# Optimization experiments

Hardware: AMD Instinct MI355X
Metric: run time of the kernel (lower is better)

## Reference

```python
import jax, jax.numpy as jnp
import numpy as np

N, C, H, W = 4, 256, 64, 64
C_EMBED = C // 2  # 128

def setup_inputs() -> dict:
    key = jax.random.key(0)
    k1, k2, k3, k4 = jax.random.split(key, 4)
    x = jax.random.normal(k1, (N, C, H, W), dtype=jnp.float32)
    # 1x1 conv weights stored as [out_ch, in_ch] (torch Conv2d weight squeezed)
    theta_w = jax.random.normal(k2, (C_EMBED, C), dtype=jnp.float32) * 0.01
    phi_w = jax.random.normal(k3, (C_EMBED, C), dtype=jnp.float32) * 0.01
    proj_w = jax.random.normal(k4, (C, C), dtype=jnp.float32) * 0.01
    return {"x": x, "theta_w": theta_w, "phi_w": phi_w, "proj_w": proj_w}

def reference(x, theta_w, phi_w, proj_w):
    n, c, h, w = x.shape
    s = h * w
    xf = x.reshape(n, c, s)  # [n, c, s]
    theta = jnp.einsum('ec,ncs->nse', theta_w, xf)  # [n, s, e]
    phi = jnp.einsum('ec,ncs->nes', phi_w, xf)      # [n, e, s]
    scale = jnp.sqrt(jnp.float32(theta_w.shape[0]))
    f = jnp.einsum('nse,net->nst', theta, phi) / scale  # [n, s, s]
    f = jax.nn.softmax(f, axis=-1)
    y = jnp.einsum('nst,nct->ncs', f, xf)  # attend over g = x, -> [n, c, s]
    res = jnp.einsum('oc,ncs->nos', proj_w, y)  # 1x1 projection conv
    return x + res.reshape(n, c, h, w)
```

## Files before the change

kernel.cpp:

```cpp
#include <hip/hip_runtime.h>
#include <cstdint>
#include <cstddef>

#define NB 4
#define CH 256
#define SS 4096
#define EE 128
#define QSCALE 0.08838834764831845f

typedef __attribute__((ext_vector_type(8))) short bfrag;
typedef __attribute__((ext_vector_type(8))) unsigned short u16x8;
typedef __attribute__((ext_vector_type(8))) _Float16 h16x8;
typedef __attribute__((ext_vector_type(4))) float f32x4;

__device__ __forceinline__ unsigned short f2bf(float f) {
  union { float f; unsigned int u; } v; v.f = f;
  unsigned int u = v.u;
  unsigned int r = u + 0x7FFFu + ((u >> 16) & 1u);
  return (unsigned short)(r >> 16);
}

__device__ __forceinline__ void lds_barrier() {
  asm volatile("s_waitcnt lgkmcnt(0)" ::: "memory");
  __builtin_amdgcn_s_barrier();
}

__global__ __launch_bounds__(256) void cvt_w(
    const float* __restrict__ thw, const float* __restrict__ phw,
    const float* __restrict__ pw,
    unsigned short* __restrict__ thwb, unsigned short* __restrict__ phwb,
    unsigned short* __restrict__ pwb)
{
  const int nw4 = EE * CH / 4;
  const int np4 = CH * CH / 4;
  int i = blockIdx.x * 256 + threadIdx.x;
  const float* src; unsigned short* dst; int off;
  if      (i < nw4)           { src = thw; dst = thwb; off = i; }
  else if (i < 2 * nw4)       { src = phw; dst = phwb; off = i - nw4; }
  else if (i < 2 * nw4 + np4) { src = pw;  dst = pwb;  off = i - 2 * nw4; }
  else return;
  float4 v = reinterpret_cast<const float4*>(src)[off];
  ushort4 o;
  o.x = f2bf(v.x); o.y = f2bf(v.y); o.z = f2bf(v.z); o.w = f2bf(v.w);
  reinterpret_cast<ushort4*>(dst)[off] = o;
}

__global__ __launch_bounds__(512) void pass1_qk(
    const float* __restrict__ x,
    const unsigned short* __restrict__ thw,
    const unsigned short* __restrict__ phw,
    unsigned short* __restrict__ xb,
    unsigned short* __restrict__ Qt,
    unsigned short* __restrict__ Kt)
{
  __shared__ unsigned short xT[64][CH + 8];
  const int t  = threadIdx.x;
  const int n  = blockIdx.y;
  const int s0 = blockIdx.x * 64;

  {
    const int soff = (t & 15) * 4;
    const int c0   = t >> 4;
    #pragma unroll
    for (int ci = 0; ci < 8; ++ci) {
      const int c = c0 + ci * 32;
      const size_t rowoff = ((size_t)n * CH + c) * SS + s0;
      float4 v = reinterpret_cast<const float4*>(x + rowoff)[soff >> 2];
      ushort4 o;
      o.x = f2bf(v.x); o.y = f2bf(v.y); o.z = f2bf(v.z); o.w = f2bf(v.w);
      reinterpret_cast<ushort4*>(xb + rowoff)[soff >> 2] = o;
      xT[soff + 0][c] = o.x;
      xT[soff + 1][c] = o.y;
      xT[soff + 2][c] = o.z;
      xT[soff + 3][c] = o.w;
    }
  }
  __syncthreads();

  const int w    = t >> 6;
  const int lane = t & 63;
  const int q    = lane >> 4;
  const int mr   = lane & 15;
  const int wrow = (w & 3) * 16;
  const int half = w >> 2;

  bfrag a[8];
  {
    const bfrag* rp = reinterpret_cast<const bfrag*>(&xT[wrow + mr][0]);
    #pragma unroll
    for (int k = 0; k < 8; ++k) a[k] = rp[k * 4 + q];
  }

  const unsigned short* wsel = half ? phw : thw;
  unsigned short*       osel = half ? Kt  : Qt;
  const float           sc   = half ? 1.0f : QSCALE;
  const bfrag* wp = reinterpret_cast<const bfrag*>(wsel);
  #pragma unroll
  for (int nt = 0; nt < 8; ++nt) {
    f32x4 acc = {0.f, 0.f, 0.f, 0.f};
    #pragma unroll
    for (int k = 0; k < 8; ++k) {
      bfrag b = wp[(nt * 16 + mr) * (CH / 8) + k * 4 + q];
      acc = __builtin_amdgcn_mfma_f32_16x16x32_bf16(a[k], b, acc, 0, 0, 0);
    }
    #pragma unroll
    for (int i = 0; i < 4; ++i) {
      const int srow = s0 + wrow + q * 4 + i;
      osel[((size_t)n * SS + srow) * EE + nt * 16 + mr] = f2bf(acc[i] * sc);
    }
  }
}

__global__ __launch_bounds__(512, 2) void pass2a(
    const unsigned short* __restrict__ Qt,
    const unsigned short* __restrict__ Kt,
    const unsigned short* __restrict__ xb,
    _Float16* __restrict__ Opart,
    float* __restrict__ ML)
{
  __shared__ __align__(16) unsigned char SMEM[103936];
  float          (*S_lds)[132] = reinterpret_cast<float(*)[132]>(SMEM);
  unsigned short (*P_lds)[136] = reinterpret_cast<unsigned short(*)[136]>(SMEM + 67584);
  float* row_m     = reinterpret_cast<float*>(SMEM + 102400);
  float* row_l     = reinterpret_cast<float*>(SMEM + 102912);
  float* row_alpha = reinterpret_cast<float*>(SMEM + 103424);

  const int t     = threadIdx.x;
  const int id    = blockIdx.x;
  const int xcd   = id & 7;
  const int n     = xcd >> 1;
  const int h     = xcd & 1;
  const int qt    = id >> 3;
  const int s0    = qt * 128;
  const int kbase = h * 2048;

  const int w      = t >> 6;
  const int lane   = t & 63;
  const int q      = lane >> 4;
  const int mr     = lane & 15;
  const int colblk = w & 3;
  const int rb     = (w >> 2) * 64;

  if (t < 128) { row_m[t] = -INFINITY; row_l[t] = 0.f; }

  bfrag qa[4][4];
  #pragma unroll
  for (int ms = 0; ms < 4; ++ms) {
    const bfrag* rp = reinterpret_cast<const bfrag*>(
        Qt + ((size_t)n * SS + s0 + rb + ms * 16 + mr) * EE);
    #pragma unroll
    for (int k = 0; k < 4; ++k) qa[ms][k] = rp[k * 4 + q];
  }

  f32x4 o_accA[4][2], o_accB[4][2];
  #pragma unroll
  for (int ms = 0; ms < 4; ++ms)
    #pragma unroll
    for (int nt = 0; nt < 2; ++nt) {
      o_accA[ms][nt] = (f32x4){0.f, 0.f, 0.f, 0.f};
      o_accB[ms][nt] = (f32x4){0.f, 0.f, 0.f, 0.f};
    }

  __syncthreads();

  bfrag kb[4][2];
  #pragma unroll
  for (int nt = 0; nt < 2; ++nt) {
    const bfrag* rp = reinterpret_cast<const bfrag*>(
        Kt + ((size_t)n * SS + kbase + colblk * 32 + nt * 16 + mr) * EE);
    #pragma unroll
    for (int k = 0; k < 4; ++k) kb[k][nt] = rp[k * 4 + q];
  }

#define PV_HALF(OACC, RB)                                                    \
  do {                                                                       \
    _Pragma("unroll")                                                        \
    for (int ms = 0; ms < 4; ++ms) {                                         \
      float al[4];                                                           \
      _Pragma("unroll")                                                      \
      for (int i = 0; i < 4; ++i) al[i] = row_alpha[(RB) + ms*16 + q*4 + i]; \
      _Pragma("unroll")                                                      \
      for (int nt = 0; nt < 2; ++nt)                                         \
        _Pragma("unroll")                                                    \
        for (int i = 0; i < 4; ++i) OACC[ms][nt][i] *= al[i];                \
    }                                                                        \
    _Pragma("unroll")                                                        \
    for (int kk = 0; kk < 4; ++kk) {                                         \
      bfrag pa[4];                                                           \
      _Pragma("unroll")                                                      \
      for (int ms = 0; ms < 4; ++ms)                                         \
        pa[ms] = reinterpret_cast<const bfrag*>(                             \
            &P_lds[(RB) + ms * 16 + mr][0])[kk * 4 + q];                     \
      _Pragma("unroll")                                                      \
      for (int nt = 0; nt < 2; ++nt)                                         \
        _Pragma("unroll")                                                    \
        for (int ms = 0; ms < 4; ++ms)                                       \
          OACC[ms][nt] = __builtin_amdgcn_mfma_f32_16x16x32_bf16(            \
              pa[ms], vb[kk][nt], OACC[ms][nt], 0, 0, 0);                    \
    }                                                                        \
  } while (0)

  for (int t0 = 0; t0 < 2048; t0 += 128) {
    bfrag vb[4][2];
    #pragma unroll
    for (int nt = 0; nt < 2; ++nt) {
      const int c = w * 32 + nt * 16 + mr;
      const bfrag* vp = reinterpret_cast<const bfrag*>(
          xb + ((size_t)n * CH + c) * SS + kbase + t0);
      #pragma unroll
      for (int kk = 0; kk < 4; ++kk) vb[kk][nt] = vp[kk * 4 + q];
    }

    #pragma unroll
    for (int ms = 0; ms < 4; ++ms) {
      f32x4 acc0 = {0.f, 0.f, 0.f, 0.f};
      f32x4 acc1 = {0.f, 0.f, 0.f, 0.f};
      #pragma unroll
      for (int k = 0; k < 4; ++k) {
        acc0 = __builtin_amdgcn_mfma_f32_16x16x32_bf16(qa[ms][k], kb[k][0], acc0, 0, 0, 0);
        acc1 = __builtin_amdgcn_mfma_f32_16x16x32_bf16(qa[ms][k], kb[k][1], acc1, 0, 0, 0);
      }
      #pragma unroll
      for (int i = 0; i < 4; ++i) {
        S_lds[rb + ms * 16 + q * 4 + i][colblk * 32 + mr]      = acc0[i];
        S_lds[rb + ms * 16 + q * 4 + i][colblk * 32 + 16 + mr] = acc1[i];
      }
    }
    lds_barrier();

    if (t0 + 128 < 2048) {
      #pragma unroll
      for (int nt = 0; nt < 2; ++nt) {
        const bfrag* rp = reinterpret_cast<const bfrag*>(
            Kt + ((size_t)n * SS + kbase + t0 + 128 + colblk * 32 + nt * 16 + mr) * EE);
        #pragma unroll
        for (int k = 0; k < 4; ++k) kb[k][nt] = rp[k * 4 + q];
      }
    }

    #pragma unroll
    for (int sh = 0; sh < 2; ++sh) {
      const int r  = sh * 64 + (t >> 3);
      const int cg = t & 7;
      const float4* srow = reinterpret_cast<const float4*>(&S_lds[r][cg * 16]);
      float4 v0 = srow[0], v1 = srow[1], v2 = srow[2], v3 = srow[3];
      float vmax = fmaxf(fmaxf(fmaxf(v0.x, v0.y), fmaxf(v0.z, v0.w)),
                         fmaxf(fmaxf(v1.x, v1.y), fmaxf(v1.z, v1.w)));
      vmax = fmaxf(vmax, fmaxf(fmaxf(fmaxf(v2.x, v2.y), fmaxf(v2.z, v2.w)),
                               fmaxf(fmaxf(v3.x, v3.y), fmaxf(v3.z, v3.w))));
      vmax = fmaxf(vmax, __shfl_xor(vmax, 1, 8));
      vmax = fmaxf(vmax, __shfl_xor(vmax, 2, 8));
      vmax = fmaxf(vmax, __shfl_xor(vmax, 4, 8));
      const float m_old = row_m[r];
      const float m_new = fmaxf(m_old, vmax);

      float p[16];
      p[0]=__expf(v0.x-m_new); p[1]=__expf(v0.y-m_new); p[2]=__expf(v0.z-m_new); p[3]=__expf(v0.w-m_new);
      p[4]=__expf(v1.x-m_new); p[5]=__expf(v1.y-m_new); p[6]=__expf(v1.z-m_new); p[7]=__expf(v1.w-m_new);
      p[8]=__expf(v2.x-m_new); p[9]=__expf(v2.y-m_new); p[10]=__expf(v2.z-m_new); p[11]=__expf(v2.w-m_new);
      p[12]=__expf(v3.x-m_new); p[13]=__expf(v3.y-m_new); p[14]=__expf(v3.z-m_new); p[15]=__expf(v3.w-m_new);
      float sum = 0.f;
      u16x8 pk0, pk1;
      #pragma unroll
      for (int j = 0; j < 8; ++j) { sum += p[j];     pk0[j] = f2bf(p[j]); }
      #pragma unroll
      for (int j = 0; j < 8; ++j) { sum += p[8 + j]; pk1[j] = f2bf(p[8 + j]); }
      *reinterpret_cast<u16x8*>(&P_lds[r][cg * 16])     = pk0;
      *reinterpret_cast<u16x8*>(&P_lds[r][cg * 16 + 8]) = pk1;
      sum += __shfl_xor(sum, 1, 8);
      sum += __shfl_xor(sum, 2, 8);
      sum += __shfl_xor(sum, 4, 8);
      if (cg == 0) {
        const float al = __expf(m_old - m_new);
        row_alpha[r] = al;
        row_m[r]     = m_new;
        row_l[r]     = row_l[r] * al + sum;
      }
    }
    lds_barrier();

    PV_HALF(o_accA, 0);
    PV_HALF(o_accB, 64);
  }

  const size_t p = ((size_t)(n * 32 + qt)) * 2 + h;

#define EPI_HALF(OACC, RB)                                                   \
  do {                                                                       \
    _Pragma("unroll")                                                        \
    for (int ms = 0; ms < 4; ++ms) {                                         \
      float inv[4];                                                          \
      _Pragma("unroll")                                                      \
      for (int i = 0; i < 4; ++i)                                            \
        inv[i] = 1.0f / row_l[(RB) + ms * 16 + q * 4 + i];                   \
      _Pragma("unroll")                                                      \
      for (int nt = 0; nt < 2; ++nt)                                         \
        _Pragma("unroll")                                                    \
        for (int i = 0; i < 4; ++i) {                                        \
          const size_t oi =                                                  \
              (p * 128 + (RB) + ms * 16 + q * 4 + i) * 256 +                 \
              w * 32 + nt * 16 + mr;                                         \
          Opart[oi] = (_Float16)(OACC[ms][nt][i] * inv[i]);                  \
        }                                                                    \
    }                                                                        \
  } while (0)

  EPI_HALF(o_accA, 0);
  EPI_HALF(o_accB, 64);
  if (t < 128) {
    ML[p * 256 + t * 2]     = row_m[t];
    ML[p * 256 + t * 2 + 1] = row_l[t];
  }
}

__global__ __launch_bounds__(512) void pass2b(
    const _Float16* __restrict__ Opart,
    const float* __restrict__ ML,
    const unsigned short* __restrict__ pwb,
    const float* __restrict__ x,
    float* __restrict__ out)
{
  __shared__ __align__(16) unsigned char SMEM[34816];
  unsigned short (*Y_lds)[CH + 8] =
      reinterpret_cast<unsigned short(*)[CH + 8]>(SMEM);
  float* w0 = reinterpret_cast<float*>(SMEM + 33792);
  float* w1 = reinterpret_cast<float*>(SMEM + 34048);

  const int t   = threadIdx.x;
  const int id  = blockIdx.x;
  const int n   = id >> 6;
  const int sub = id & 63;
  const int s0  = sub * 64;
  const int qt  = sub >> 1;
  const int rb  = (sub & 1) * 64;
  const size_t p0 = ((size_t)(n * 32 + qt)) * 2;

  if (t < 64) {
    const float ma = ML[p0 * 256 + (rb + t) * 2];
    const float la = ML[p0 * 256 + (rb + t) * 2 + 1];
    const float mb = ML[(p0 + 1) * 256 + (rb + t) * 2];
    const float lb = ML[(p0 + 1) * 256 + (rb + t) * 2 + 1];
    const float m  = fmaxf(ma, mb);
    const float e0 = __expf(ma - m) * la;
    const float e1 = __expf(mb - m) * lb;
    const float iL = 1.0f / (e0 + e1);
    w0[t] = e0 * iL;
    w1[t] = e1 * iL;
  }
  __syncthreads();

  {
    const int r = t >> 3;
    #pragma unroll
    for (int seg = 0; seg < 4; ++seg) {
      const int c0 = (t & 7) * 8 + seg * 64;
      const size_t ai = (p0 * 128 + rb + r) * 256 + c0;
      const size_t bi = ((p0 + 1) * 128 + rb + r) * 256 + c0;
      h16x8 ha = *reinterpret_cast<const h16x8*>(Opart + ai);
      h16x8 hb = *reinterpret_cast<const h16x8*>(Opart + bi);
      u16x8 y;
      #pragma unroll
      for (int j = 0; j < 8; ++j)
        y[j] = f2bf((float)ha[j] * w0[r] + (float)hb[j] * w1[r]);
      *reinterpret_cast<u16x8*>(&Y_lds[r][c0]) = y;
    }
  }
  __syncthreads();

  const int w    = t >> 6;
  const int lane = t & 63;
  const int q    = lane >> 4;
  const int mr   = lane & 15;
  #pragma unroll
  for (int ot = 0; ot < 2; ++ot) {
    const int o0 = w * 32 + ot * 16;
    bfrag a[8];
    {
      const bfrag* ap = reinterpret_cast<const bfrag*>(pwb + (o0 + mr) * CH);
      #pragma unroll
      for (int k = 0; k < 8; ++k) a[k] = ap[k * 4 + q];
    }
    #pragma unroll
    for (int st = 0; st < 4; ++st) {
      f32x4 acc = {0.f, 0.f, 0.f, 0.f};
      const bfrag* bp = reinterpret_cast<const bfrag*>(&Y_lds[st * 16 + mr][0]);
      #pragma unroll
      for (int k = 0; k < 8; ++k)
        acc = __builtin_amdgcn_mfma_f32_16x16x32_bf16(a[k], bp[k * 4 + q], acc, 0, 0, 0);
      #pragma unroll
      for (int i = 0; i < 4; ++i) {
        const int o = o0 + q * 4 + i;
        const int s = s0 + st * 16 + mr;
        const size_t idx = ((size_t)n * CH + o) * SS + s;
        out[idx] = x[idx] + acc[i];
      }
    }
  }
}

__global__ __launch_bounds__(512, 2) void pass2_full(
    const unsigned short* __restrict__ Qt,
    const unsigned short* __restrict__ Kt,
    const unsigned short* __restrict__ xb,
    const unsigned short* __restrict__ pwb,
    const float* __restrict__ x,
    float* __restrict__ out)
{
  __shared__ __align__(16) unsigned char SMEM[51968];
  float          (*S_lds)[132] = reinterpret_cast<float(*)[132]>(SMEM);
  unsigned short (*P_lds)[136] = reinterpret_cast<unsigned short(*)[136]>(SMEM + 33792);
  float* row_m     = reinterpret_cast<float*>(SMEM + 51200);
  float* row_l     = reinterpret_cast<float*>(SMEM + 51456);
  float* row_alpha = reinterpret_cast<float*>(SMEM + 51712);

  const int t    = threadIdx.x;
  const int id   = blockIdx.x;
  const int xcd  = id & 7;
  const int n    = xcd >> 1;
  const int s0   = ((id >> 3) * 2 + (xcd & 1)) * 64;
  const int w    = t >> 6;
  const int lane = t & 63;
  const int q    = lane >> 4;
  const int mr   = lane & 15;

  if (t < 64) { row_m[t] = -INFINITY; row_l[t] = 0.f; }

  bfrag qa[4][4];
  #pragma unroll
  for (int ms = 0; ms < 4; ++ms) {
    const bfrag* rp = reinterpret_cast<const bfrag*>(
        Qt + ((size_t)n * SS + s0 + ms * 16 + mr) * EE);
    #pragma unroll
    for (int k = 0; k < 4; ++k) qa[ms][k] = rp[k * 4 + q];
  }

  f32x4 o_acc[4][2];
  #pragma unroll
  for (int ms = 0; ms < 4; ++ms)
    #pragma unroll
    for (int nt = 0; nt < 2; ++nt) o_acc[ms][nt] = (f32x4){0.f, 0.f, 0.f, 0.f};

  bfrag kb[4];
  {
    const bfrag* rp = reinterpret_cast<const bfrag*>(
        Kt + ((size_t)n * SS + w * 16 + mr) * EE);
    #pragma unroll
    for (int k = 0; k < 4; ++k) kb[k] = rp[k * 4 + q];
  }

  for (int t0 = 0; t0 < SS; t0 += 128) {
    bfrag vb[4][2];
    #pragma unroll
    for (int nt = 0; nt < 2; ++nt) {
      const int c = w * 32 + nt * 16 + mr;
      const bfrag* vp = reinterpret_cast<const bfrag*>(
          xb + ((size_t)n * CH + c) * SS + t0);
      #pragma unroll
      for (int kk = 0; kk < 4; ++kk) vb[kk][nt] = vp[kk * 4 + q];
    }

    #pragma unroll
    for (int ms = 0; ms < 4; ++ms) {
      f32x4 acc = {0.f, 0.f, 0.f, 0.f};
      #pragma unroll
      for (int k = 0; k < 4; ++k)
        acc = __builtin_amdgcn_mfma_f32_16x16x32_bf16(qa[ms][k], kb[k], acc, 0, 0, 0);
      #pragma unroll
      for (int i = 0; i < 4; ++i)
        S_lds[ms * 16 + q * 4 + i][w * 16 + mr] = acc[i];
    }
    lds_barrier();

    {
      const int t1 = t0 + 128;
      if (t1 < SS) {
        const bfrag* rp = reinterpret_cast<const bfrag*>(
            Kt + ((size_t)n * SS + t1 + w * 16 + mr) * EE);
        #pragma unroll
        for (int k = 0; k < 4; ++k) kb[k] = rp[k * 4 + q];
      }
    }

    {
      const int r  = t >> 3;
      const int cg = t & 7;
      const float4* srow = reinterpret_cast<const float4*>(&S_lds[r][cg * 16]);
      float4 v0 = srow[0], v1 = srow[1], v2 = srow[2], v3 = srow[3];
      float vmax = fmaxf(fmaxf(fmaxf(v0.x, v0.y), fmaxf(v0.z, v0.w)),
                         fmaxf(fmaxf(v1.x, v1.y), fmaxf(v1.z, v1.w)));
      vmax = fmaxf(vmax, fmaxf(fmaxf(fmaxf(v2.x, v2.y), fmaxf(v2.z, v2.w)),
                               fmaxf(fmaxf(v3.x, v3.y), fmaxf(v3.z, v3.w))));
      vmax = fmaxf(vmax, __shfl_xor(vmax, 1, 8));
      vmax = fmaxf(vmax, __shfl_xor(vmax, 2, 8));
      vmax = fmaxf(vmax, __shfl_xor(vmax, 4, 8));
      const float m_old = row_m[r];
      const float m_new = fmaxf(m_old, vmax);

      float p[16];
      p[0]=__expf(v0.x-m_new); p[1]=__expf(v0.y-m_new); p[2]=__expf(v0.z-m_new); p[3]=__expf(v0.w-m_new);
      p[4]=__expf(v1.x-m_new); p[5]=__expf(v1.y-m_new); p[6]=__expf(v1.z-m_new); p[7]=__expf(v1.w-m_new);
      p[8]=__expf(v2.x-m_new); p[9]=__expf(v2.y-m_new); p[10]=__expf(v2.z-m_new); p[11]=__expf(v2.w-m_new);
      p[12]=__expf(v3.x-m_new); p[13]=__expf(v3.y-m_new); p[14]=__expf(v3.z-m_new); p[15]=__expf(v3.w-m_new);
      float sum = 0.f;
      u16x8 pk0, pk1;
      #pragma unroll
      for (int j = 0; j < 8; ++j) { sum += p[j];     pk0[j] = f2bf(p[j]); }
      #pragma unroll
      for (int j = 0; j < 8; ++j) { sum += p[8 + j]; pk1[j] = f2bf(p[8 + j]); }
      *reinterpret_cast<u16x8*>(&P_lds[r][cg * 16])     = pk0;
      *reinterpret_cast<u16x8*>(&P_lds[r][cg * 16 + 8]) = pk1;
      sum += __shfl_xor(sum, 1, 8);
      sum += __shfl_xor(sum, 2, 8);
      sum += __shfl_xor(sum, 4, 8);
      if (cg == 0) {
        const float al = __expf(m_old - m_new);
        row_alpha[r] = al;
        row_m[r]     = m_new;
        row_l[r]     = row_l[r] * al + sum;
      }
    }
    lds_barrier();

    #pragma unroll
    for (int ms = 0; ms < 4; ++ms) {
      float al[4];
      #pragma unroll
      for (int i = 0; i < 4; ++i) al[i] = row_alpha[ms * 16 + q * 4 + i];
      #pragma unroll
      for (int nt = 0; nt < 2; ++nt)
        #pragma unroll
        for (int i = 0; i < 4; ++i) o_acc[ms][nt][i] *= al[i];
    }

    #pragma unroll
    for (int kk = 0; kk < 4; ++kk) {
      bfrag pa[4];
      #pragma unroll
      for (int ms = 0; ms < 4; ++ms)
        pa[ms] = reinterpret_cast<const bfrag*>(&P_lds[ms * 16 + mr][0])[kk * 4 + q];
      #pragma unroll
      for (int nt = 0; nt < 2; ++nt)
        #pragma unroll
        for (int ms = 0; ms < 4; ++ms)
          o_acc[ms][nt] = __builtin_amdgcn_mfma_f32_16x16x32_bf16(
              pa[ms], vb[kk][nt], o_acc[ms][nt], 0, 0, 0);
    }
  }

  __syncthreads();
  unsigned short (*Y_lds)[CH + 8] =
      reinterpret_cast<unsigned short(*)[CH + 8]>(SMEM);

  #pragma unroll
  for (int ms = 0; ms < 4; ++ms) {
    float inv[4];
    #pragma unroll
    for (int i = 0; i < 4; ++i) inv[i] = 1.0f / row_l[ms * 16 + q * 4 + i];
    #pragma unroll
    for (int nt = 0; nt < 2; ++nt) {
      const int c = w * 32 + nt * 16 + mr;
      #pragma unroll
      for (int i = 0; i < 4; ++i)
        Y_lds[ms * 16 + q * 4 + i][c] = f2bf(o_acc[ms][nt][i] * inv[i]);
    }
  }
  __syncthreads();

  #pragma unroll
  for (int ot = 0; ot < 2; ++ot) {
    const int o0 = w * 32 + ot * 16;
    bfrag a[8];
    {
      const bfrag* ap = reinterpret_cast<const bfrag*>(pwb + (o0 + mr) * CH);
      #pragma unroll
      for (int k = 0; k < 8; ++k) a[k] = ap[k * 4 + q];
    }
    #pragma unroll
    for (int st = 0; st < 4; ++st) {
      f32x4 acc = {0.f, 0.f, 0.f, 0.f};
      const bfrag* bp = reinterpret_cast<const bfrag*>(&Y_lds[st * 16 + mr][0]);
      #pragma unroll
      for (int k = 0; k < 8; ++k)
        acc = __builtin_amdgcn_mfma_f32_16x16x32_bf16(a[k], bp[k * 4 + q], acc, 0, 0, 0);
      #pragma unroll
      for (int i = 0; i < 4; ++i) {
        const int o = o0 + q * 4 + i;
        const int s = s0 + st * 16 + mr;
        const size_t idx = ((size_t)n * CH + o) * SS + s;
        out[idx] = x[idx] + acc[i];
      }
    }
  }
}

extern "C" void kernel_launch(void* const* d_in, const int* in_sizes, int n_in,
                              void* d_out, int out_size, void* d_ws, size_t ws_size,
                              hipStream_t stream) {
  const float* x   = (const float*)d_in[0];
  const float* thw = (const float*)d_in[1];
  const float* phw = (const float*)d_in[2];
  const float* pw  = (const float*)d_in[3];
  float* out = (float*)d_out;

  unsigned short* xb   = (unsigned short*)d_ws;
  unsigned short* Qt   = xb + (size_t)NB * CH * SS;
  unsigned short* Kt   = Qt + (size_t)NB * SS * EE;
  unsigned short* thwb = Kt + (size_t)NB * SS * EE;
  unsigned short* phwb = thwb + EE * CH;
  unsigned short* pwb  = phwb + EE * CH;
  float*          ML   = (float*)(pwb + CH * CH);
  _Float16*       Opart = (_Float16*)(ML + (size_t)256 * 128 * 2);

  const size_t opart_off = (size_t)((char*)Opart - (char*)d_ws);
  const size_t opart_bytes = (size_t)256 * 128 * 256 * 2;
  const int fits = ws_size >= opart_off + opart_bytes;

  const int nw4 = EE * CH / 4;
  const int np4 = CH * CH / 4;
  const int totw4 = 2 * nw4 + np4;
  cvt_w<<<(totw4 + 255) / 256, 256, 0, stream>>>(thw, phw, pw, thwb, phwb, pwb);

  pass1_qk<<<dim3(SS / 64, NB), 512, 0, stream>>>(x, thwb, phwb, xb, Qt, Kt);

  if (fits) {
    pass2a<<<dim3(256), 512, 0, stream>>>(Qt, Kt, xb, Opart, ML);
    pass2b<<<dim3(256), 512, 0, stream>>>(Opart, ML, pwb, x, out);
  } else {
    pass2_full<<<dim3(NB * SS / 64), 512, 0, stream>>>(Qt, Kt, xb, pwb, x, out);
  }
}
```

Before: 191.8 us.

## Split attention keys into quarters, stage Q/K in LDS, store scores as bf16

The flash-attention pass now splits the key range into four quarters instead of two, so it launches 512 blocks instead of 256. Q and K tiles are staged in LDS, with K double-buffered through registers, and the key step shrinks from 128 to 64. Scores are written to LDS as bf16 in a buffer shared with P, which cuts LDS use enough to allow higher occupancy (launch bounds 4). The combine kernel merges four partial results, which doubles the Opart workspace and its traffic, and rounding scores to bf16 before softmax costs accuracy.

```diff
diff --git a/kernel.cpp b/kernel.cpp
--- a/kernel.cpp
+++ b/kernel.cpp
@@ -18,6 +18,10 @@
   unsigned int u = v.u;
   unsigned int r = u + 0x7FFFu + ((u >> 16) & 1u);
   return (unsigned short)(r >> 16);
+}
+__device__ __forceinline__ float bf2f(unsigned short u) {
+  union { unsigned int u; float f; } v; v.u = ((unsigned int)u) << 16;
+  return v.f;
 }
 
 __device__ __forceinline__ void lds_barrier() {
@@ -111,45 +115,57 @@
   }
 }
 
-__global__ __launch_bounds__(512, 2) void pass2a(
+__global__ __launch_bounds__(512, 4) void pass2a(
     const unsigned short* __restrict__ Qt,
     const unsigned short* __restrict__ Kt,
     const unsigned short* __restrict__ xb,
     _Float16* __restrict__ Opart,
     float* __restrict__ ML)
 {
-  __shared__ __align__(16) unsigned char SMEM[103936];
-  float          (*S_lds)[132] = reinterpret_cast<float(*)[132]>(SMEM);
-  unsigned short (*P_lds)[136] = reinterpret_cast<unsigned short(*)[136]>(SMEM + 67584);
-  float* row_m     = reinterpret_cast<float*>(SMEM + 102400);
-  float* row_l     = reinterpret_cast<float*>(SMEM + 102912);
-  float* row_alpha = reinterpret_cast<float*>(SMEM + 103424);
-
-  const int t     = threadIdx.x;
-  const int id    = blockIdx.x;
-  const int xcd   = id & 7;
-  const int n     = xcd >> 1;
-  const int h     = xcd & 1;
-  const int qt    = id >> 3;
-  const int s0    = qt * 128;
-  const int kbase = h * 2048;
-
-  const int w      = t >> 6;
-  const int lane   = t & 63;
-  const int q      = lane >> 4;
-  const int mr     = lane & 15;
-  const int colblk = w & 3;
-  const int rb     = (w >> 2) * 64;
+  __shared__ __align__(16) unsigned char SMEM[69632];
+  unsigned short (*Q_lds)[132] = reinterpret_cast<unsigned short(*)[132]>(SMEM);
+  unsigned short (*SP)[68]     = reinterpret_cast<unsigned short(*)[68]>(SMEM + 33792);
+  unsigned short (*K_lds)[132] = reinterpret_cast<unsigned short(*)[132]>(SMEM + 51200);
+  float* row_m     = reinterpret_cast<float*>(SMEM + 68096);
+  float* row_l     = reinterpret_cast<float*>(SMEM + 68608);
+  float* row_alpha = reinterpret_cast<float*>(SMEM + 69120);
+
+  const int t       = threadIdx.x;
+  const int id      = blockIdx.x;
+  const int xcd     = id & 7;
+  const int n       = xcd >> 1;
+  const int quarter = (xcd & 1) * 2 + ((id >> 3) & 1);
+  const int qt      = id >> 4;
+  const int s0      = qt * 128;
+  const int kq0     = quarter * 1024;
+
+  const int w    = t >> 6;
+  const int lane = t & 63;
+  const int q    = lane >> 4;
+  const int mr   = lane & 15;
+  const int rb   = (w >> 2) * 64;
+  const int c4   = w & 3;
 
   if (t < 128) { row_m[t] = -INFINITY; row_l[t] = 0.f; }
 
-  bfrag qa[4][4];
-  #pragma unroll
-  for (int ms = 0; ms < 4; ++ms) {
-    const bfrag* rp = reinterpret_cast<const bfrag*>(
-        Qt + ((size_t)n * SS + s0 + rb + ms * 16 + mr) * EE);
-    #pragma unroll
-    for (int k = 0; k < 4; ++k) qa[ms][k] = rp[k * 4 + q];
+  {
+    const int r  = t >> 2;
+    const int j0 = (t & 3) * 4;
+    const unsigned short* src = Qt + ((size_t)n * SS + s0 + r) * EE;
+    #pragma unroll
+    for (int j = 0; j < 4; ++j) {
+      const int col = (j0 + j) * 8;
+      *reinterpret_cast<u16x8*>(&Q_lds[r][col]) =
+          *reinterpret_cast<const u16x8*>(src + col);
+    }
+  }
+  {
+    const int key = t >> 3, c = t & 7;
+    const unsigned short* src = Kt + ((size_t)n * SS + kq0 + key) * EE;
+    *reinterpret_cast<u16x8*>(&K_lds[key][c * 8]) =
+        *reinterpret_cast<const u16x8*>(src + c * 8);
+    *reinterpret_cast<u16x8*>(&K_lds[key][(c + 8) * 8]) =
+        *reinterpret_cast<const u16x8*>(src + (c + 8) * 8);
   }
 
   f32x4 o_accA[4][2], o_accB[4][2];
@@ -162,15 +178,6 @@
     }
 
   __syncthreads();
-
-  bfrag kb[4][2];
-  #pragma unroll
-  for (int nt = 0; nt < 2; ++nt) {
-    const bfrag* rp = reinterpret_cast<const bfrag*>(
-        Kt + ((size_t)n * SS + kbase + colblk * 32 + nt * 16 + mr) * EE);
-    #pragma unroll
-    for (int k = 0; k < 4; ++k) kb[k][nt] = rp[k * 4 + q];
-  }
 
 #define PV_HALF(OACC, RB)                                                    \
   do {                                                                       \
@@ -185,12 +192,12 @@
         for (int i = 0; i < 4; ++i) OACC[ms][nt][i] *= al[i];                \
     }                                                                        \
     _Pragma("unroll")                                                        \
-    for (int kk = 0; kk < 4; ++kk) {                                         \
+    for (int kk = 0; kk < 2; ++kk) {                                         \
       bfrag pa[4];                                                           \
       _Pragma("unroll")                                                      \
       for (int ms = 0; ms < 4; ++ms)                                         \
-        pa[ms] = reinterpret_cast<const bfrag*>(                             \
-            &P_lds[(RB) + ms * 16 + mr][0])[kk * 4 + q];                     \
+        pa[ms] = *reinterpret_cast<const bfrag*>(                            \
+            &SP[(RB) + ms * 16 + mr][(kk * 4 + q) * 8]);                     \
       _Pragma("unroll")                                                      \
       for (int nt = 0; nt < 2; ++nt)                                         \
         _Pragma("unroll")                                                    \
@@ -200,76 +207,78 @@
     }                                                                        \
   } while (0)
 
-  for (int t0 = 0; t0 < 2048; t0 += 128) {
-    bfrag vb[4][2];
+  for (int t0 = 0; t0 < 1024; t0 += 64) {
+    bfrag vb[2][2];
     #pragma unroll
     for (int nt = 0; nt < 2; ++nt) {
       const int c = w * 32 + nt * 16 + mr;
       const bfrag* vp = reinterpret_cast<const bfrag*>(
-          xb + ((size_t)n * CH + c) * SS + kbase + t0);
-      #pragma unroll
-      for (int kk = 0; kk < 4; ++kk) vb[kk][nt] = vp[kk * 4 + q];
-    }
-
-    #pragma unroll
-    for (int ms = 0; ms < 4; ++ms) {
-      f32x4 acc0 = {0.f, 0.f, 0.f, 0.f};
-      f32x4 acc1 = {0.f, 0.f, 0.f, 0.f};
-      #pragma unroll
-      for (int k = 0; k < 4; ++k) {
-        acc0 = __builtin_amdgcn_mfma_f32_16x16x32_bf16(qa[ms][k], kb[k][0], acc0, 0, 0, 0);
-        acc1 = __builtin_amdgcn_mfma_f32_16x16x32_bf16(qa[ms][k], kb[k][1], acc1, 0, 0, 0);
-      }
-      #pragma unroll
-      for (int i = 0; i < 4; ++i) {
-        S_lds[rb + ms * 16 + q * 4 + i][colblk * 32 + mr]      = acc0[i];
-        S_lds[rb + ms * 16 + q * 4 + i][colblk * 32 + 16 + mr] = acc1[i];
+          xb + ((size_t)n * CH + c) * SS + kq0 + t0);
+      vb[0][nt] = vp[q];
+      vb[1][nt] = vp[4 + q];
+    }
+
+    {
+      bfrag kb[4];
+      #pragma unroll
+      for (int k = 0; k < 4; ++k)
+        kb[k] = *reinterpret_cast<const bfrag*>(
+            &K_lds[c4 * 16 + mr][(k * 4 + q) * 8]);
+      #pragma unroll
+      for (int ms = 0; ms < 4; ++ms) {
+        f32x4 acc = {0.f, 0.f, 0.f, 0.f};
+        #pragma unroll
+        for (int k = 0; k < 4; ++k) {
+          bfrag aq = *reinterpret_cast<const bfrag*>(
+              &Q_lds[rb + ms * 16 + mr][(k * 4 + q) * 8]);
+          acc = __builtin_amdgcn_mfma_f32_16x16x32_bf16(aq, kb[k], acc, 0, 0, 0);
+        }
+        #pragma unroll
+        for (int i = 0; i < 4; ++i)
+          SP[rb + ms * 16 + q * 4 + i][c4 * 16 + mr] = f2bf(acc[i]);
       }
     }
     lds_barrier();
 
-    if (t0 + 128 < 2048) {
-      #pragma unroll
-      for (int nt = 0; nt < 2; ++nt) {
-        const bfrag* rp = reinterpret_cast<const bfrag*>(
-            Kt + ((size_t)n * SS + kbase + t0 + 128 + colblk * 32 + nt * 16 + mr) * EE);
-        #pragma unroll
-        for (int k = 0; k < 4; ++k) kb[k][nt] = rp[k * 4 + q];
-      }
-    }
-
-    #pragma unroll
-    for (int sh = 0; sh < 2; ++sh) {
-      const int r  = sh * 64 + (t >> 3);
-      const int cg = t & 7;
-      const float4* srow = reinterpret_cast<const float4*>(&S_lds[r][cg * 16]);
-      float4 v0 = srow[0], v1 = srow[1], v2 = srow[2], v3 = srow[3];
-      float vmax = fmaxf(fmaxf(fmaxf(v0.x, v0.y), fmaxf(v0.z, v0.w)),
-                         fmaxf(fmaxf(v1.x, v1.y), fmaxf(v1.z, v1.w)));
-      vmax = fmaxf(vmax, fmaxf(fmaxf(fmaxf(v2.x, v2.y), fmaxf(v2.z, v2.w)),
-                               fmaxf(fmaxf(v3.x, v3.y), fmaxf(v3.z, v3.w))));
-      vmax = fmaxf(vmax, __shfl_xor(vmax, 1, 8));
-      vmax = fmaxf(vmax, __shfl_xor(vmax, 2, 8));
-      vmax = fmaxf(vmax, __shfl_xor(vmax, 4, 8));
+    u16x8 kr0, kr1;
+    const bool pf = (t0 + 64) < 1024;
+    if (pf) {
+      const int key = t >> 3, c = t & 7;
+      const unsigned short* src =
+          Kt + ((size_t)n * SS + kq0 + t0 + 64 + key) * EE;
+      kr0 = *reinterpret_cast<const u16x8*>(src + c * 8);
+      kr1 = *reinterpret_cast<const u16x8*>(src + (c + 8) * 8);
+    }
+
+    {
+      const int r  = t >> 2;
+      const int cg = t & 3;
+      u16x8 sv0 = *reinterpret_cast<const u16x8*>(&SP[r][cg * 16]);
+      u16x8 sv1 = *reinterpret_cast<const u16x8*>(&SP[r][cg * 16 + 8]);
+      float s[16];
+      #pragma unroll
+      for (int j = 0; j < 8; ++j) { s[j] = bf2f(sv0[j]); s[8 + j] = bf2f(sv1[j]); }
+      float vmax = s[0];
+      #pragma unroll
+      for (int j = 1; j < 16; ++j) vmax = fmaxf(vmax, s[j]);
+      vmax = fmaxf(vmax, __shfl_xor(vmax, 1, 4));
+      vmax = fmaxf(vmax, __shfl_xor(vmax, 2, 4));
       const float m_old = row_m[r];
       const float m_new = fmaxf(m_old, vmax);
-
-      float p[16];
-      p[0]=__expf(v0.x-m_new); p[1]=__expf(v0.y-m_new); p[2]=__expf(v0.z-m_new); p[3]=__expf(v0.w-m_new);
-      p[4]=__expf(v1.x-m_new); p[5]=__expf(v1.y-m_new); p[6]=__expf(v1.z-m_new); p[7]=__expf(v1.w-m_new);
-      p[8]=__expf(v2.x-m_new); p[9]=__expf(v2.y-m_new); p[10]=__expf(v2.z-m_new); p[11]=__expf(v2.w-m_new);
-      p[12]=__expf(v3.x-m_new); p[13]=__expf(v3.y-m_new); p[14]=__expf(v3.z-m_new); p[15]=__expf(v3.w-m_new);
       float sum = 0.f;
       u16x8 pk0, pk1;
       #pragma unroll
-      for (int j = 0; j < 8; ++j) { sum += p[j];     pk0[j] = f2bf(p[j]); }
-      #pragma unroll
-      for (int j = 0; j < 8; ++j) { sum += p[8 + j]; pk1[j] = f2bf(p[8 + j]); }
-      *reinterpret_cast<u16x8*>(&P_lds[r][cg * 16])     = pk0;
-      *reinterpret_cast<u16x8*>(&P_lds[r][cg * 16 + 8]) = pk1;
-      sum += __shfl_xor(sum, 1, 8);
-      sum += __shfl_xor(sum, 2, 8);
-      sum += __shfl_xor(sum, 4, 8);
+      for (int j = 0; j < 8; ++j) {
+        float p = __expf(s[j] - m_new); sum += p; pk0[j] = f2bf(p);
+      }
+      #pragma unroll
+      for (int j = 0; j < 8; ++j) {
+        float p = __expf(s[8 + j] - m_new); sum += p; pk1[j] = f2bf(p);
+      }
+      *reinterpret_cast<u16x8*>(&SP[r][cg * 16])     = pk0;
+      *reinterpret_cast<u16x8*>(&SP[r][cg * 16 + 8]) = pk1;
+      sum += __shfl_xor(sum, 1, 4);
+      sum += __shfl_xor(sum, 2, 4);
       if (cg == 0) {
         const float al = __expf(m_old - m_new);
         row_alpha[r] = al;
@@ -281,9 +290,16 @@
 
     PV_HALF(o_accA, 0);
     PV_HALF(o_accB, 64);
-  }
-
-  const size_t p = ((size_t)(n * 32 + qt)) * 2 + h;
+
+    if (pf) {
+      const int key = t >> 3, c = t & 7;
+      *reinterpret_cast<u16x8*>(&K_lds[key][c * 8])       = kr0;
+      *reinterpret_cast<u16x8*>(&K_lds[key][(c + 8) * 8]) = kr1;
+    }
+    lds_barrier();
+  }
+
+  const size_t p = ((size_t)(n * 32 + qt)) * 4 + quarter;
 
 #define EPI_HALF(OACC, RB)                                                   \
   do {                                                                       \
@@ -323,8 +339,7 @@
   __shared__ __align__(16) unsigned char SMEM[34816];
   unsigned short (*Y_lds)[CH + 8] =
       reinterpret_cast<unsigned short(*)[CH + 8]>(SMEM);
-  float* w0 = reinterpret_cast<float*>(SMEM + 33792);
-  float* w1 = reinterpret_cast<float*>(SMEM + 34048);
+  float (*W)[64] = reinterpret_cast<float(*)[64]>(SMEM + 33792);
 
   const int t   = threadIdx.x;
   const int id  = blockIdx.x;
@@ -333,19 +348,22 @@
   const int s0  = sub * 64;
   const int qt  = sub >> 1;
   const int rb  = (sub & 1) * 64;
-  const size_t p0 = ((size_t)(n * 32 + qt)) * 2;
+  const size_t p0 = ((size_t)(n * 32 + qt)) * 4;
 
   if (t < 64) {
-    const float ma = ML[p0 * 256 + (rb + t) * 2];
-    const float la = ML[p0 * 256 + (rb + t) * 2 + 1];
-    const float mb = ML[(p0 + 1) * 256 + (rb + t) * 2];
-    const float lb = ML[(p0 + 1) * 256 + (rb + t) * 2 + 1];
-    const float m  = fmaxf(ma, mb);
-    const float e0 = __expf(ma - m) * la;
-    const float e1 = __expf(mb - m) * lb;
-    const float iL = 1.0f / (e0 + e1);
-    w0[t] = e0 * iL;
-    w1[t] = e1 * iL;
+    float m[4], l[4];
+    #pragma unroll
+    for (int qi = 0; qi < 4; ++qi) {
+      m[qi] = ML[(p0 + qi) * 256 + (rb + t) * 2];
+      l[qi] = ML[(p0 + qi) * 256 + (rb + t) * 2 + 1];
+    }
+    const float mm = fmaxf(fmaxf(m[0], m[1]), fmaxf(m[2], m[3]));
+    float e[4], se = 0.f;
+    #pragma unroll
+    for (int qi = 0; qi < 4; ++qi) { e[qi] = __expf(m[qi] - mm) * l[qi]; se += e[qi]; }
+    const float iL = 1.0f / se;
+    #pragma unroll
+    for (int qi = 0; qi < 4; ++qi) W[qi][t] = e[qi] * iL;
   }
   __syncthreads();
 
@@ -354,14 +372,18 @@
     #pragma unroll
     for (int seg = 0; seg < 4; ++seg) {
       const int c0 = (t & 7) * 8 + seg * 64;
-      const size_t ai = (p0 * 128 + rb + r) * 256 + c0;
-      const size_t bi = ((p0 + 1) * 128 + rb + r) * 256 + c0;
-      h16x8 ha = *reinterpret_cast<const h16x8*>(Opart + ai);
-      h16x8 hb = *reinterpret_cast<const h16x8*>(Opart + bi);
+      float acc[8] = {0.f, 0.f, 0.f, 0.f, 0.f, 0.f, 0.f, 0.f};
+      #pragma unroll
+      for (int qi = 0; qi < 4; ++qi) {
+        h16x8 hv = *reinterpret_cast<const h16x8*>(
+            Opart + ((p0 + qi) * 128 + rb + r) * 256 + c0);
+        const float wq = W[qi][r];
+        #pragma unroll
+        for (int j = 0; j < 8; ++j) acc[j] += (float)hv[j] * wq;
+      }
       u16x8 y;
       #pragma unroll
-      for (int j = 0; j < 8; ++j)
-        y[j] = f2bf((float)ha[j] * w0[r] + (float)hb[j] * w1[r]);
+      for (int j = 0; j < 8; ++j) y[j] = f2bf(acc[j]);
       *reinterpret_cast<u16x8*>(&Y_lds[r][c0]) = y;
     }
   }
@@ -609,10 +631,10 @@
   unsigned short* phwb = thwb + EE * CH;
   unsigned short* pwb  = phwb + EE * CH;
   float*          ML   = (float*)(pwb + CH * CH);
-  _Float16*       Opart = (_Float16*)(ML + (size_t)256 * 128 * 2);
-
-  const size_t opart_off = (size_t)((char*)Opart - (char*)d_ws);
-  const size_t opart_bytes = (size_t)256 * 128 * 256 * 2;
+  _Float16*       Opart = (_Float16*)(ML + (size_t)512 * 256);
+
+  const size_t opart_off  = (size_t)((char*)Opart - (char*)d_ws);
+  const size_t opart_bytes = (size_t)512 * 128 * 256 * 2;
   const int fits = ws_size >= opart_off + opart_bytes;
 
   const int nw4 = EE * CH / 4;
@@ -623,7 +645,7 @@
   pass1_qk<<<dim3(SS / 64, NB), 512, 0, stream>>>(x, thwb, phwb, xb, Qt, Kt);
 
   if (fits) {
-    pass2a<<<dim3(256), 512, 0, stream>>>(Qt, Kt, xb, Opart, ML);
+    pass2a<<<dim3(512), 512, 0, stream>>>(Qt, Kt, xb, Opart, ML);
     pass2b<<<dim3(256), 512, 0, stream>>>(Opart, ML, pwb, x, out);
   } else {
     pass2_full<<<dim3(NB * SS / 64), 512, 0, stream>>>(Qt, Kt, xb, pwb, x, out);
```

Result: slower. 425.8 us (+122.0%).

## Restructure attention pass to per-wave query rows with register softmax and LDS-staged V

Applied to the files above, without the earlier changes.

Reworks the flash-attention kernel so each wave owns 16 query rows and computes S transposed (K·Q) in registers. Row max, exp and sum are then done with cross-lane shuffles instead of round-tripping S and P through LDS. P fragments are rearranged into MFMA A-operand layout with shuffles. V (x) tiles of 64 keys are double-buffered in a swizzled LDS layout with a global prefetch, and there is one barrier per step instead of two. This cuts LDS traffic and synchronisation, at the cost of each wave reloading K from global memory, more MFMA steps with smaller key tiles, and 16 accumulator tiles of register pressure per wave.

```diff
diff --git a/kernel.cpp b/kernel.cpp
--- a/kernel.cpp
+++ b/kernel.cpp
@@ -18,6 +18,9 @@
   unsigned int u = v.u;
   unsigned int r = u + 0x7FFFu + ((u >> 16) & 1u);
   return (unsigned short)(r >> 16);
+}
+__device__ __forceinline__ unsigned int packbf(float a, float b) {
+  return (unsigned int)f2bf(a) | ((unsigned int)f2bf(b) << 16);
 }
 
 __device__ __forceinline__ void lds_barrier() {
@@ -118,12 +121,7 @@
     _Float16* __restrict__ Opart,
     float* __restrict__ ML)
 {
-  __shared__ __align__(16) unsigned char SMEM[103936];
-  float          (*S_lds)[132] = reinterpret_cast<float(*)[132]>(SMEM);
-  unsigned short (*P_lds)[136] = reinterpret_cast<unsigned short(*)[136]>(SMEM + 67584);
-  float* row_m     = reinterpret_cast<float*>(SMEM + 102400);
-  float* row_l     = reinterpret_cast<float*>(SMEM + 102912);
-  float* row_alpha = reinterpret_cast<float*>(SMEM + 103424);
+  __shared__ __align__(16) unsigned char SMEM[65536];
 
   const int t     = threadIdx.x;
   const int id    = blockIdx.x;
@@ -134,182 +132,174 @@
   const int s0    = qt * 128;
   const int kbase = h * 2048;
 
-  const int w      = t >> 6;
-  const int lane   = t & 63;
-  const int q      = lane >> 4;
-  const int mr     = lane & 15;
-  const int colblk = w & 3;
-  const int rb     = (w >> 2) * 64;
-
-  if (t < 128) { row_m[t] = -INFINITY; row_l[t] = 0.f; }
-
-  bfrag qa[4][4];
+  const int w    = t >> 6;
+  const int lane = t & 63;
+  const int q    = lane >> 4;
+  const int mr   = lane & 15;
+  const int qs0  = w * 16;
+
+  bfrag qf[4];
+  {
+    const bfrag* rp = reinterpret_cast<const bfrag*>(
+        Qt + ((size_t)n * SS + s0 + qs0 + mr) * EE);
+    #pragma unroll
+    for (int kk = 0; kk < 4; ++kk) qf[kk] = rp[kk * 4 + q];
+  }
+
+  f32x4 o_acc[16];
   #pragma unroll
-  for (int ms = 0; ms < 4; ++ms) {
-    const bfrag* rp = reinterpret_cast<const bfrag*>(
-        Qt + ((size_t)n * SS + s0 + rb + ms * 16 + mr) * EE);
-    #pragma unroll
-    for (int k = 0; k < 4; ++k) qa[ms][k] = rp[k * 4 + q];
-  }
-
-  f32x4 o_accA[4][2], o_accB[4][2];
-  #pragma unroll
-  for (int ms = 0; ms < 4; ++ms)
-    #pragma unroll
-    for (int nt = 0; nt < 2; ++nt) {
-      o_accA[ms][nt] = (f32x4){0.f, 0.f, 0.f, 0.f};
-      o_accB[ms][nt] = (f32x4){0.f, 0.f, 0.f, 0.f};
-    }
-
+  for (int cb = 0; cb < 16; ++cb) o_acc[cb] = (f32x4){0.f, 0.f, 0.f, 0.f};
+  float m_run = -INFINITY;
+  float l_run = 0.f;
+
+  {
+    const int chunk = t & 7;
+    #pragma unroll
+    for (int rep = 0; rep < 4; ++rep) {
+      const int ch = (t >> 3) + rep * 64;
+      u16x8 v = *reinterpret_cast<const u16x8*>(
+          xb + ((size_t)n * CH + ch) * SS + kbase + chunk * 8);
+      *reinterpret_cast<u16x8*>(
+          SMEM + ch * 128 + ((chunk * 16) ^ ((ch & 7) << 4))) = v;
+    }
+  }
   __syncthreads();
 
-  bfrag kb[4][2];
-  #pragma unroll
-  for (int nt = 0; nt < 2; ++nt) {
-    const bfrag* rp = reinterpret_cast<const bfrag*>(
-        Kt + ((size_t)n * SS + kbase + colblk * 32 + nt * 16 + mr) * EE);
-    #pragma unroll
-    for (int k = 0; k < 4; ++k) kb[k][nt] = rp[k * 4 + q];
-  }
-
-#define PV_HALF(OACC, RB)                                                    \
-  do {                                                                       \
-    _Pragma("unroll")                                                        \
-    for (int ms = 0; ms < 4; ++ms) {                                         \
-      float al[4];                                                           \
-      _Pragma("unroll")                                                      \
-      for (int i = 0; i < 4; ++i) al[i] = row_alpha[(RB) + ms*16 + q*4 + i]; \
-      _Pragma("unroll")                                                      \
-      for (int nt = 0; nt < 2; ++nt)                                         \
-        _Pragma("unroll")                                                    \
-        for (int i = 0; i < 4; ++i) OACC[ms][nt][i] *= al[i];                \
-    }                                                                        \
-    _Pragma("unroll")                                                        \
-    for (int kk = 0; kk < 4; ++kk) {                                         \
-      bfrag pa[4];                                                           \
-      _Pragma("unroll")                                                      \
-      for (int ms = 0; ms < 4; ++ms)                                         \
-        pa[ms] = reinterpret_cast<const bfrag*>(                             \
-            &P_lds[(RB) + ms * 16 + mr][0])[kk * 4 + q];                     \
-      _Pragma("unroll")                                                      \
-      for (int nt = 0; nt < 2; ++nt)                                         \
-        _Pragma("unroll")                                                    \
-        for (int ms = 0; ms < 4; ++ms)                                       \
-          OACC[ms][nt] = __builtin_amdgcn_mfma_f32_16x16x32_bf16(            \
-              pa[ms], vb[kk][nt], OACC[ms][nt], 0, 0, 0);                    \
-    }                                                                        \
-  } while (0)
-
-  for (int t0 = 0; t0 < 2048; t0 += 128) {
-    bfrag vb[4][2];
-    #pragma unroll
-    for (int nt = 0; nt < 2; ++nt) {
-      const int c = w * 32 + nt * 16 + mr;
-      const bfrag* vp = reinterpret_cast<const bfrag*>(
-          xb + ((size_t)n * CH + c) * SS + kbase + t0);
-      #pragma unroll
-      for (int kk = 0; kk < 4; ++kk) vb[kk][nt] = vp[kk * 4 + q];
-    }
-
-    #pragma unroll
-    for (int ms = 0; ms < 4; ++ms) {
-      f32x4 acc0 = {0.f, 0.f, 0.f, 0.f};
-      f32x4 acc1 = {0.f, 0.f, 0.f, 0.f};
-      #pragma unroll
-      for (int k = 0; k < 4; ++k) {
-        acc0 = __builtin_amdgcn_mfma_f32_16x16x32_bf16(qa[ms][k], kb[k][0], acc0, 0, 0, 0);
-        acc1 = __builtin_amdgcn_mfma_f32_16x16x32_bf16(qa[ms][k], kb[k][1], acc1, 0, 0, 0);
-      }
+  const int srcA = mr + ((2 * (q & 1)) << 4);
+  const int srcB = srcA + 16;
+  const bool hi  = (q >> 1) != 0;
+
+  for (int t0 = 0; t0 < 2048; t0 += 64) {
+    unsigned char* Vcur = SMEM + ((t0 >> 6) & 1) * 32768;
+    unsigned char* Vnxt = SMEM + (((t0 >> 6) + 1) & 1) * 32768;
+    const bool pf = (t0 + 64) < 2048;
+
+    u16x8 gr[4];
+    if (pf) {
+      const int chunk = t & 7;
+      #pragma unroll
+      for (int rep = 0; rep < 4; ++rep) {
+        const int ch = (t >> 3) + rep * 64;
+        gr[rep] = *reinterpret_cast<const u16x8*>(
+            xb + ((size_t)n * CH + ch) * SS + kbase + t0 + 64 + chunk * 8);
+      }
+    }
+
+    f32x4 s[4];
+    {
+      bfrag kf[4][4];
+      #pragma unroll
+      for (int kb = 0; kb < 4; ++kb) {
+        const bfrag* rp = reinterpret_cast<const bfrag*>(
+            Kt + ((size_t)n * SS + kbase + t0 + kb * 16 + mr) * EE);
+        #pragma unroll
+        for (int kk = 0; kk < 4; ++kk) kf[kb][kk] = rp[kk * 4 + q];
+      }
+      #pragma unroll
+      for (int kb = 0; kb < 4; ++kb) {
+        f32x4 acc = {0.f, 0.f, 0.f, 0.f};
+        #pragma unroll
+        for (int kk = 0; kk < 4; ++kk)
+          acc = __builtin_amdgcn_mfma_f32_16x16x32_bf16(kf[kb][kk], qf[kk], acc, 0, 0, 0);
+        s[kb] = acc;
+      }
+    }
+
+    float vmax = s[0][0];
+    #pragma unroll
+    for (int kb = 0; kb < 4; ++kb)
+      #pragma unroll
+      for (int i = 0; i < 4; ++i) vmax = fmaxf(vmax, s[kb][i]);
+    vmax = fmaxf(vmax, __shfl_xor(vmax, 16, 64));
+    vmax = fmaxf(vmax, __shfl_xor(vmax, 32, 64));
+    const float m_new = fmaxf(m_run, vmax);
+    const float alpha = __expf(m_run - m_new);
+    float sum = 0.f;
+    unsigned int dw[4][2];
+    #pragma unroll
+    for (int kb = 0; kb < 4; ++kb) {
+      float p0 = __expf(s[kb][0] - m_new);
+      float p1 = __expf(s[kb][1] - m_new);
+      float p2 = __expf(s[kb][2] - m_new);
+      float p3 = __expf(s[kb][3] - m_new);
+      sum += (p0 + p1) + (p2 + p3);
+      dw[kb][0] = packbf(p0, p1);
+      dw[kb][1] = packbf(p2, p3);
+    }
+    sum += __shfl_xor(sum, 16, 64);
+    sum += __shfl_xor(sum, 32, 64);
+    l_run = l_run * alpha + sum;
+    m_run = m_new;
+
+    {
+      float al[4];
+      #pragma unroll
+      for (int i = 0; i < 4; ++i) al[i] = __shfl(alpha, q * 4 + i, 64);
+      #pragma unroll
+      for (int cb = 0; cb < 16; ++cb)
+        #pragma unroll
+        for (int i = 0; i < 4; ++i) o_acc[cb][i] *= al[i];
+    }
+
+    bfrag pa[2];
+    #pragma unroll
+    for (int kkp = 0; kkp < 2; ++kkp) {
+      int a00 = __shfl((int)dw[2 * kkp + 0][0], srcA, 64);
+      int a01 = __shfl((int)dw[2 * kkp + 0][1], srcA, 64);
+      int a10 = __shfl((int)dw[2 * kkp + 1][0], srcA, 64);
+      int a11 = __shfl((int)dw[2 * kkp + 1][1], srcA, 64);
+      int b00 = __shfl((int)dw[2 * kkp + 0][0], srcB, 64);
+      int b01 = __shfl((int)dw[2 * kkp + 0][1], srcB, 64);
+      int b10 = __shfl((int)dw[2 * kkp + 1][0], srcB, 64);
+      int b11 = __shfl((int)dw[2 * kkp + 1][1], srcB, 64);
+      union { int v[4]; bfrag b; } cv;
+      cv.v[0] = hi ? a10 : a00;
+      cv.v[1] = hi ? a11 : a01;
+      cv.v[2] = hi ? b10 : b00;
+      cv.v[3] = hi ? b11 : b01;
+      pa[kkp] = cv.b;
+    }
+
+    #pragma unroll
+    for (int cb = 0; cb < 16; ++cb) {
+      const int ch = cb * 16 + mr;
+      bfrag vf0 = *reinterpret_cast<const bfrag*>(
+          Vcur + ch * 128 + ((q * 16) ^ ((ch & 7) << 4)));
+      bfrag vf1 = *reinterpret_cast<const bfrag*>(
+          Vcur + ch * 128 + ((64 + q * 16) ^ ((ch & 7) << 4)));
+      o_acc[cb] = __builtin_amdgcn_mfma_f32_16x16x32_bf16(pa[0], vf0, o_acc[cb], 0, 0, 0);
+      o_acc[cb] = __builtin_amdgcn_mfma_f32_16x16x32_bf16(pa[1], vf1, o_acc[cb], 0, 0, 0);
+    }
+
+    if (pf) {
+      const int chunk = t & 7;
+      #pragma unroll
+      for (int rep = 0; rep < 4; ++rep) {
+        const int ch = (t >> 3) + rep * 64;
+        *reinterpret_cast<u16x8*>(
+            Vnxt + ch * 128 + ((chunk * 16) ^ ((ch & 7) << 4))) = gr[rep];
+      }
+    }
+    lds_barrier();
+  }
+
+  const size_t p = ((size_t)(n * 32 + qt)) * 2 + h;
+  {
+    const float linv = 1.0f / l_run;
+    float invl[4];
+    #pragma unroll
+    for (int i = 0; i < 4; ++i) invl[i] = __shfl(linv, q * 4 + i, 64);
+    #pragma unroll
+    for (int cb = 0; cb < 16; ++cb)
       #pragma unroll
       for (int i = 0; i < 4; ++i) {
-        S_lds[rb + ms * 16 + q * 4 + i][colblk * 32 + mr]      = acc0[i];
-        S_lds[rb + ms * 16 + q * 4 + i][colblk * 32 + 16 + mr] = acc1[i];
-      }
-    }
-    lds_barrier();
-
-    if (t0 + 128 < 2048) {
-      #pragma unroll
-      for (int nt = 0; nt < 2; ++nt) {
-        const bfrag* rp = reinterpret_cast<const bfrag*>(
-            Kt + ((size_t)n * SS + kbase + t0 + 128 + colblk * 32 + nt * 16 + mr) * EE);
-        #pragma unroll
-        for (int k = 0; k < 4; ++k) kb[k][nt] = rp[k * 4 + q];
-      }
-    }
-
-    #pragma unroll
-    for (int sh = 0; sh < 2; ++sh) {
-      const int r  = sh * 64 + (t >> 3);
-      const int cg = t & 7;
-      const float4* srow = reinterpret_cast<const float4*>(&S_lds[r][cg * 16]);
-      float4 v0 = srow[0], v1 = srow[1], v2 = srow[2], v3 = srow[3];
-      float vmax = fmaxf(fmaxf(fmaxf(v0.x, v0.y), fmaxf(v0.z, v0.w)),
-                         fmaxf(fmaxf(v1.x, v1.y), fmaxf(v1.z, v1.w)));
-      vmax = fmaxf(vmax, fmaxf(fmaxf(fmaxf(v2.x, v2.y), fmaxf(v2.z, v2.w)),
-                               fmaxf(fmaxf(v3.x, v3.y), fmaxf(v3.z, v3.w))));
-      vmax = fmaxf(vmax, __shfl_xor(vmax, 1, 8));
-      vmax = fmaxf(vmax, __shfl_xor(vmax, 2, 8));
-      vmax = fmaxf(vmax, __shfl_xor(vmax, 4, 8));
-      const float m_old = row_m[r];
-      const float m_new = fmaxf(m_old, vmax);
-
-      float p[16];
-      p[0]=__expf(v0.x-m_new); p[1]=__expf(v0.y-m_new); p[2]=__expf(v0.z-m_new); p[3]=__expf(v0.w-m_new);
-      p[4]=__expf(v1.x-m_new); p[5]=__expf(v1.y-m_new); p[6]=__expf(v1.z-m_new); p[7]=__expf(v1.w-m_new);
-      p[8]=__expf(v2.x-m_new); p[9]=__expf(v2.y-m_new); p[10]=__expf(v2.z-m_new); p[11]=__expf(v2.w-m_new);
-      p[12]=__expf(v3.x-m_new); p[13]=__expf(v3.y-m_new); p[14]=__expf(v3.z-m_new); p[15]=__expf(v3.w-m_new);
-      float sum = 0.f;
-      u16x8 pk0, pk1;
-      #pragma unroll
-      for (int j = 0; j < 8; ++j) { sum += p[j];     pk0[j] = f2bf(p[j]); }
-      #pragma unroll
-      for (int j = 0; j < 8; ++j) { sum += p[8 + j]; pk1[j] = f2bf(p[8 + j]); }
-      *reinterpret_cast<u16x8*>(&P_lds[r][cg * 16])     = pk0;
-      *reinterpret_cast<u16x8*>(&P_lds[r][cg * 16 + 8]) = pk1;
-      sum += __shfl_xor(sum, 1, 8);
-      sum += __shfl_xor(sum, 2, 8);
-      sum += __shfl_xor(sum, 4, 8);
-      if (cg == 0) {
-        const float al = __expf(m_old - m_new);
-        row_alpha[r] = al;
-        row_m[r]     = m_new;
-        row_l[r]     = row_l[r] * al + sum;
-      }
-    }
-    lds_barrier();
-
-    PV_HALF(o_accA, 0);
-    PV_HALF(o_accB, 64);
-  }
-
-  const size_t p = ((size_t)(n * 32 + qt)) * 2 + h;
-
-#define EPI_HALF(OACC, RB)                                                   \
-  do {                                                                       \
-    _Pragma("unroll")                                                        \
-    for (int ms = 0; ms < 4; ++ms) {                                         \
-      float inv[4];                                                          \
-      _Pragma("unroll")                                                      \
-      for (int i = 0; i < 4; ++i)                                            \
-        inv[i] = 1.0f / row_l[(RB) + ms * 16 + q * 4 + i];                   \
-      _Pragma("unroll")                                                      \
-      for (int nt = 0; nt < 2; ++nt)                                         \
-        _Pragma("unroll")                                                    \
-        for (int i = 0; i < 4; ++i) {                                        \
-          const size_t oi =                                                  \
-              (p * 128 + (RB) + ms * 16 + q * 4 + i) * 256 +                 \
-              w * 32 + nt * 16 + mr;                                         \
-          Opart[oi] = (_Float16)(OACC[ms][nt][i] * inv[i]);                  \
-        }                                                                    \
-    }                                                                        \
-  } while (0)
-
-  EPI_HALF(o_accA, 0);
-  EPI_HALF(o_accB, 64);
-  if (t < 128) {
-    ML[p * 256 + t * 2]     = row_m[t];
-    ML[p * 256 + t * 2 + 1] = row_l[t];
+        const size_t oi = (p * 128 + qs0 + q * 4 + i) * 256 + cb * 16 + mr;
+        Opart[oi] = (_Float16)(o_acc[cb][i] * invl[i]);
+      }
+  }
+  if (lane < 16) {
+    ML[p * 256 + (qs0 + lane) * 2]     = m_run;
+    ML[p * 256 + (qs0 + lane) * 2 + 1] = l_run;
   }
 }
 
```

New measurement: 285.8 us. +49.0%, slower.
